# Performance work log

Hardware: AMD Instinct MI355X
Metric: run time of the kernel (lower is better)

Reference implementation:

```python
import jax, jax.numpy as jnp
import numpy as np

LAMBDA_W = 1.0
NEG_INF = -1e10


def setup_inputs() -> dict:
    key = jax.random.key(0)
    k1, k2, k3 = jax.random.split(key, 3)
    B, L, D = 8, 2048, 256
    h_x = jax.random.normal(k1, (B, L, D), dtype=jnp.float32)
    h_y = jax.random.normal(k2, (B, L, D), dtype=jnp.float32)
    # masks: valid prefix of 3/4 length, padded tail of zeros (exercises masking)
    valid = (3 * L) // 4
    base = (jnp.arange(L) < valid).astype(jnp.float32)
    x_mask = jnp.broadcast_to(base, (B, L))
    y_mask = jnp.broadcast_to(base, (B, L))
    # biaffine weight (n_label=1, no biases), init_value scaling kept at O(1)
    W = jax.random.normal(k3, (D, D), dtype=jnp.float32) / jnp.sqrt(jnp.float32(D))
    return {"h_x": h_x, "h_y": h_y, "x_mask": x_mask, "y_mask": y_mask, "W": W}


def reference(h_x, h_y, x_mask, y_mask, W):
    # src = h_x [B,Ls,D], pred = h_y [B,Lp,D]
    src, pred = h_x, h_y
    src_mask, pred_mask = x_mask, y_mask

    # cost_mx[b,p,s] = ||src[b,s] - pred[b,p]||_2, via ||a||^2+||b||^2-2ab
    src_sq = jnp.sum(src * src, axis=-1)            # [B,Ls]
    pred_sq = jnp.sum(pred * pred, axis=-1)         # [B,Lp]
    cross = jnp.einsum('bpd,bsd->bps', pred, src)   # [B,Lp,Ls]
    cost_mx = jnp.sqrt(jnp.maximum(pred_sq[:, :, None] + src_sq[:, None, :] - 2.0 * cross, 0.0))

    # biaffine scores: pred W src^T  -> [B,Lp,Ls]
    tr_mx = jnp.einsum('bpd,de,bse->bps', pred, W, src)

    # cost_mask[b,p,s] = pred_mask[b,p]*src_mask[b,s]
    cost_mask = pred_mask[:, :, None] * src_mask[:, None, :]
    tr_mx = jnp.where(cost_mask == 0, NEG_INF, tr_mx)
    tr_prob = jax.nn.softmax(tr_mx, axis=-1)

    flow_cost = tr_prob * cost_mx                   # [B,Lp,Ls]

    nL1 = jnp.sum(pred_mask, axis=-1, keepdims=True)  # [B,1]
    nL2 = jnp.sum(src_mask, axis=-1, keepdims=True)   # [B,1]
    fc = jnp.sum(flow_cost, axis=(1, 2), keepdims=True)  # [B,1,1]
    fc = fc / (nL1 * nL2)   # broadcasts [B,1,1]/[B,1] -> [B,B,1], matches torch
    fc = jnp.mean(fc)
    return fc * LAMBDA_W
```

## Files before the change

kernel.cpp:

```cpp
#include <hip/hip_runtime.h>
#include <math.h>
#include <stdint.h>

#define B_ 8
#define L_ 2048
#define D_ 256
#define NEG_INF_V (-1e10f)
#define NSTRIP 32

typedef __bf16 bf16x8 __attribute__((ext_vector_type(8)));
typedef float f32x4 __attribute__((ext_vector_type(4)));

#define MFMA16(a, b, c) __builtin_amdgcn_mfma_f32_16x16x32_bf16((a), (b), (c), 0, 0, 0)


__global__ __launch_bounds__(256) void convert_kernel(
    const float* __restrict__ x, const float* __restrict__ y,
    const float* __restrict__ W,
    __bf16* __restrict__ srcFM, __bf16* __restrict__ predFM,
    __bf16* __restrict__ WFM,
    float* __restrict__ src_sq, float* __restrict__ pred_sq) {
    int tid = threadIdx.x;
    int blk = blockIdx.x;
    if (blk < 2048) {
        const float* in = (blk < 1024) ? x : y;
        __bf16* out = (blk < 1024) ? srcFM : predFM;
        float* sqout = (blk < 1024) ? src_sq : pred_sq;
        int g = blk & 1023;
        __shared__ __align__(16) __bf16 sFM[512 * 8];
        __shared__ float sSQ[16];
        int kb = (tid & 31) >> 2, qq = tid & 3;
        #pragma unroll
        for (int pass = 0; pass < 2; ++pass) {
            int m = pass * 8 + (tid >> 5);
            const float* p = in + ((size_t)g * 16 + m) * D_ + (tid & 31) * 8;
            float4 v0 = *(const float4*)p;
            float4 v1 = *(const float4*)(p + 4);
            float ss = v0.x * v0.x + v0.y * v0.y + v0.z * v0.z + v0.w * v0.w +
                       v1.x * v1.x + v1.y * v1.y + v1.z * v1.z + v1.w * v1.w;
            #pragma unroll
            for (int o = 16; o > 0; o >>= 1) ss += __shfl_xor(ss, o, 64);
            if ((tid & 31) == 0) sSQ[m] = ss;
            union { __bf16 o[8]; bf16x8 v; } cv;
            cv.o[0] = (__bf16)v0.x; cv.o[1] = (__bf16)v0.y;
            cv.o[2] = (__bf16)v0.z; cv.o[3] = (__bf16)v0.w;
            cv.o[4] = (__bf16)v1.x; cv.o[5] = (__bf16)v1.y;
            cv.o[6] = (__bf16)v1.z; cv.o[7] = (__bf16)v1.w;
            *(bf16x8*)(sFM + (m * 32 + kb * 4 + qq) * 8) = cv.v;
        }
        __syncthreads();
        int G0 = tid * 2;
        int kb0 = G0 >> 6, q0 = (G0 >> 4) & 3, m0 = G0 & 15;
        bf16x8 a = *(const bf16x8*)(sFM + (m0 * 32 + kb0 * 4 + q0) * 8);
        bf16x8 bgr = *(const bf16x8*)(sFM + ((m0 + 1) * 32 + kb0 * 4 + q0) * 8);
        *(bf16x8*)(out + ((size_t)g * 512 + G0) * 8) = a;
        *(bf16x8*)(out + ((size_t)g * 512 + G0 + 1) * 8) = bgr;
        if (tid < 16) sqout[g * 16 + tid] = sSQ[tid];
    } else {
        int idx = (blk - 2048) * 256 + tid;
        int m = idx & 15, q = (idx >> 4) & 3, kb = (idx >> 6) & 7, gn = idx >> 9;
        union { __bf16 o[8]; bf16x8 v; } cv;
        #pragma unroll
        for (int j = 0; j < 8; ++j)
            cv.o[j] = (__bf16)W[(size_t)(kb * 32 + q * 8 + j) * D_ + gn * 16 + m];
        *(bf16x8*)(WFM + (size_t)idx * 8) = cv.v;
    }
}

__global__ __launch_bounds__(256, 2) void predw_mfma(
    const __bf16* __restrict__ predFM, const __bf16* __restrict__ WFM,
    const float* __restrict__ pred_mask, __bf16* __restrict__ pwFM) {
    __shared__ __align__(16) __bf16 sT[128 * 136];
    __shared__ int flag;
    int tid = threadIdx.x, lane = tid & 63, wid = tid >> 6;
    int wp = wid >> 1, wn = wid & 1;
    int id = blockIdx.x;
    int m0 = (((id >> 3) & 15) + (id & 7) * 16) * 128;
    int n0 = (id >> 7) * 128;
    if (tid == 0) flag = 0;
    __syncthreads();
    if (tid < 128) { if (pred_mask[m0 + tid] != 0.f) atomicOr(&flag, 1); }
    __syncthreads();
    if (!flag) return;

    const __bf16* bA = predFM + (size_t)(m0 / 16 + wp * 4) * 4096 + lane * 8;
    const __bf16* bB = WFM + (size_t)(n0 / 16 + wn * 4) * 4096 + lane * 8;
    f32x4 acc[4][4] = {};
    #pragma unroll
    for (int kb = 0; kb < 8; ++kb) {
        bf16x8 fA[4], fB[4];
        #pragma unroll
        for (int t = 0; t < 4; ++t) {
            fA[t] = *(const bf16x8*)(bA + (t * 8 + kb) * 512);
            fB[t] = *(const bf16x8*)(bB + (t * 8 + kb) * 512);
        }
        #pragma unroll
        for (int pt = 0; pt < 4; ++pt)
            #pragma unroll
            for (int st = 0; st < 4; ++st)
                acc[pt][st] = MFMA16(fA[pt], fB[st], acc[pt][st]);
    }
    int q = lane >> 4, cn = lane & 15;
    #pragma unroll
    for (int pt = 0; pt < 4; ++pt)
        #pragma unroll
        for (int st = 0; st < 4; ++st)
            #pragma unroll
            for (int r = 0; r < 4; ++r)
                sT[(wp * 64 + pt * 16 + q * 4 + r) * 136 + wn * 64 + st * 16 + cn] =
                    (__bf16)acc[pt][st][r];
    __syncthreads();
    #pragma unroll
    for (int i = 0; i < 8; ++i) {
        int idx = i * 256 + tid;
        int gl = idx >> 8, kbl = (idx >> 6) & 3, qq = (idx >> 4) & 3, mm = idx & 15;
        bf16x8 v = *(const bf16x8*)(sT + (gl * 16 + mm) * 136 + kbl * 32 + qq * 8);
        *(bf16x8*)(pwFM +
                   (((size_t)(m0 / 16 + gl) * 8 + n0 / 32 + kbl) * 64 + qq * 16 + mm) * 8) = v;
    }
}

__global__ __launch_bounds__(256, 4) void fused_mfma(
    const __bf16* __restrict__ srcFM, const __bf16* __restrict__ predFM,
    const __bf16* __restrict__ pwFM,
    const float* __restrict__ src_mask, const float* __restrict__ pred_mask,
    const float* __restrict__ src_sq, const float* __restrict__ pred_sq,
    float* __restrict__ m_part, float* __restrict__ l_part,
    float* __restrict__ w_part, float* __restrict__ Sarr,
    unsigned int* __restrict__ counter) {
    __shared__ __align__(16) __bf16 sS[64 * 256];
    __shared__ float sPM[128], sPSQ[128], sSM[64], sSSQ[64];
    __shared__ int flg[4];
    int tid = threadIdx.x, lane = tid & 63, wid = tid >> 6;
    int id = blockIdx.x;
    int b = id & 7, px = (id >> 3) & 15, syb = id >> 7;
    int p0 = px * 128, s0 = syb * 64;

    if (id == 0) {
        if (tid == 0) *counter = 0u;
        if (tid < 24) Sarr[tid] = 0.f;
    }
    if (tid < 4) flg[tid] = 0;
    __syncthreads();
    if (tid < 128) {
        float v = pred_mask[b * L_ + p0 + tid];
        sPM[tid] = v;
        sPSQ[tid] = pred_sq[b * L_ + p0 + tid];
        atomicOr(&flg[(v != 0.f) ? 0 : 1], 1);
    } else if (tid < 192) {
        int t = tid - 128;
        float v = src_mask[b * L_ + s0 + t];
        sSM[t] = v;
        sSSQ[t] = src_sq[b * L_ + s0 + t];
        atomicOr(&flg[(v != 0.f) ? 2 : 3], 1);
    }
    {
        const __bf16* g = srcFM + ((size_t)(b * 128 + syb * 4)) * 4096;
        #pragma unroll
        for (int i = 0; i < 8; ++i) {
            size_t off = (size_t)i * 2048 + tid * 8;
            *(bf16x8*)(sS + off) = *(const bf16x8*)(g + off);
        }
    }
    __syncthreads();
    const bool anyVP = flg[0] != 0, anyIP = flg[1] != 0, anyVS = flg[2] != 0;
    const bool doT = anyVP && anyVS;
    const bool doG = anyVS || anyIP;
    if (!doG) {
        if (tid < 128) {
            size_t o = (size_t)syb * (B_ * L_) + b * L_ + p0 + tid;
            m_part[o] = NEG_INF_V; l_part[o] = 64.f; w_part[o] = 0.f;
        }
        return;
    }

    const __bf16* bP = predFM + ((size_t)(b * 128 + px * 8 + wid * 2)) * 4096 + lane * 8;
    const __bf16* bW = pwFM + ((size_t)(b * 128 + px * 8 + wid * 2)) * 4096 + lane * 8;
    const __bf16* bS = sS + lane * 8;

    f32x4 aG[2][4] = {};
    f32x4 aT[2][4] = {};
    if (doT) {
        #pragma unroll
        for (int kb = 0; kb < 8; ++kb) {
            bf16x8 fP[2], fW[2], fB[4];
            #pragma unroll
            for (int m = 0; m < 2; ++m) {
                fP[m] = *(const bf16x8*)(bP + (m * 8 + kb) * 512);
                fW[m] = *(const bf16x8*)(bW + (m * 8 + kb) * 512);
            }
            #pragma unroll
            for (int t = 0; t < 4; ++t)
                fB[t] = *(const bf16x8*)(bS + (t * 8 + kb) * 512);
            #pragma unroll
            for (int m = 0; m < 2; ++m)
                #pragma unroll
                for (int t = 0; t < 4; ++t) {
                    aG[m][t] = MFMA16(fP[m], fB[t], aG[m][t]);
                    aT[m][t] = MFMA16(fW[m], fB[t], aT[m][t]);
                }
        }
    } else {
        #pragma unroll
        for (int kb = 0; kb < 8; ++kb) {
            bf16x8 fP[2], fB[4];
            #pragma unroll
            for (int m = 0; m < 2; ++m)
                fP[m] = *(const bf16x8*)(bP + (m * 8 + kb) * 512);
            #pragma unroll
            for (int t = 0; t < 4; ++t)
                fB[t] = *(const bf16x8*)(bS + (t * 8 + kb) * 512);
            #pragma unroll
            for (int m = 0; m < 2; ++m)
                #pragma unroll
                for (int t = 0; t < 4; ++t)
                    aG[m][t] = MFMA16(fP[m], fB[t], aG[m][t]);
        }
    }

    int q = lane >> 4, cn = lane & 15;
    float smv[4], sqv[4];
    #pragma unroll
    for (int t = 0; t < 4; ++t) {
        smv[t] = sSM[t * 16 + cn];
        sqv[t] = sSSQ[t * 16 + cn];
    }
    #pragma unroll
    for (int m = 0; m < 2; ++m) {
        int rbase = wid * 32 + m * 16 + q * 4;
        #pragma unroll
        for (int r = 0; r < 4; ++r) {
            float pm = sPM[rbase + r], psq = sPSQ[rbase + r];
            float tv[4], cst[4];
            float tm = -1e30f;
            #pragma unroll
            for (int t = 0; t < 4; ++t) {
                cst[t] = __builtin_amdgcn_sqrtf(
                    fmaxf(psq + sqv[t] - 2.f * aG[m][t][r], 0.f));
                float tt = doT ? aT[m][t][r] : NEG_INF_V;
                tv[t] = (pm == 0.f) ? 0.f : (smv[t] != 0.f ? tt : NEG_INF_V);
                tm = fmaxf(tm, tv[t]);
            }
            #pragma unroll
            for (int o = 8; o > 0; o >>= 1) tm = fmaxf(tm, __shfl_xor(tm, o, 16));
            float l = 0.f, w = 0.f;
            #pragma unroll
            for (int t = 0; t < 4; ++t) {
                float e = __expf(tv[t] - tm);
                l += e;
                w = fmaf(e, cst[t], w);
            }
            #pragma unroll
            for (int o = 8; o > 0; o >>= 1) {
                l += __shfl_xor(l, o, 16);
                w += __shfl_xor(w, o, 16);
            }
            if (cn == 0) {
                size_t o = (size_t)syb * (B_ * L_) + b * L_ + p0 + rbase + r;
                m_part[o] = tm;
                l_part[o] = l;
                w_part[o] = w;
            }
        }
    }
}

__global__ __launch_bounds__(256) void combine_kernel(
    const float* __restrict__ m_part, const float* __restrict__ l_part,
    const float* __restrict__ w_part,
    const float* __restrict__ x_mask, const float* __restrict__ y_mask,
    float* __restrict__ Sarr, unsigned int* __restrict__ counter,
    float* __restrict__ out) {
    int tid = threadIdx.x;
    int r = blockIdx.x * 256 + tid;
    int b = r >> 11;
    float mm = -1e30f;
    #pragma unroll
    for (int s = 0; s < NSTRIP; ++s) mm = fmaxf(mm, m_part[(size_t)s * (B_ * L_) + r]);
    float l = 0.f, w = 0.f;
    #pragma unroll
    for (int s = 0; s < NSTRIP; ++s) {
        size_t o = (size_t)s * (B_ * L_) + r;
        float e = __expf(m_part[o] - mm);
        l = fmaf(l_part[o], e, l);
        w = fmaf(w_part[o], e, w);
    }
    float sv = w / l;
    float n1 = y_mask[r], n2 = x_mask[r];
    __shared__ float red[3][256];
    red[0][tid] = sv; red[1][tid] = n1; red[2][tid] = n2;
    __syncthreads();
    for (int o = 128; o > 0; o >>= 1) {
        if (tid < o) {
            red[0][tid] += red[0][tid + o];
            red[1][tid] += red[1][tid + o];
            red[2][tid] += red[2][tid + o];
        }
        __syncthreads();
    }
    __shared__ int isLast;
    if (tid == 0) {
        atomicAdd(&Sarr[b], red[0][0]);
        atomicAdd(&Sarr[8 + b], red[1][0]);
        atomicAdd(&Sarr[16 + b], red[2][0]);
        __threadfence();
        isLast = (atomicAdd(counter, 1u) == 63u) ? 1 : 0;
    }
    __syncthreads();
    if (isLast) {
        __shared__ float fb[24];
        if (tid < 24) fb[tid] = atomicAdd(&Sarr[tid], 0.f);
        __syncthreads();
        if (tid == 0) {
            float ss = 0.f, si = 0.f;
            for (int bb = 0; bb < B_; bb++) {
                ss += fb[bb];
                si += 1.0f / (fb[8 + bb] * fb[16 + bb]);
            }
            out[0] = ss * si / (float)(B_ * B_);
        }
    }
}

extern "C" void kernel_launch(void* const* d_in, const int* in_sizes, int n_in,
                              void* d_out, int out_size, void* d_ws, size_t ws_size,
                              hipStream_t stream) {
    const float* h_x = (const float*)d_in[0];
    const float* h_y = (const float*)d_in[1];
    const float* x_mask = (const float*)d_in[2];
    const float* y_mask = (const float*)d_in[3];
    const float* W = (const float*)d_in[4];

    char* w8 = (char*)d_ws;
    const size_t BLD2 = (size_t)B_ * L_ * D_ * 2;
    __bf16* srcFM = (__bf16*)w8;
    __bf16* predFM = (__bf16*)(w8 + BLD2);
    __bf16* pwFM = (__bf16*)(w8 + 2 * BLD2);
    __bf16* WFM = (__bf16*)(w8 + 3 * BLD2);
    float* src_sq = (float*)(w8 + 3 * BLD2 + (1 << 17));
    float* pred_sq = (float*)(w8 + 3 * BLD2 + (1 << 17) + (1 << 16));
    char* pbase = w8 + 3 * BLD2 + (1 << 17) + (1 << 17);
    const size_t PSZ = (size_t)B_ * L_ * NSTRIP * 4;
    float* m_part = (float*)pbase;
    float* l_part = (float*)(pbase + PSZ);
    float* w_part = (float*)(pbase + 2 * PSZ);
    float* Sarr = (float*)(pbase + 3 * PSZ);
    unsigned int* counter = (unsigned int*)(pbase + 3 * PSZ + 128);

    convert_kernel<<<2080, 256, 0, stream>>>(h_x, h_y, W, srcFM, predFM, WFM,
                                             src_sq, pred_sq);
    predw_mfma<<<256, 256, 0, stream>>>(predFM, WFM, y_mask, pwFM);
    fused_mfma<<<4096, 256, 0, stream>>>(
        srcFM, predFM, pwFM, x_mask, y_mask, src_sq, pred_sq,
        m_part, l_part, w_part, Sarr, counter);
    combine_kernel<<<B_ * L_ / 256, 256, 0, stream>>>(
        m_part, l_part, w_part, x_mask, y_mask, Sarr, counter, (float*)d_out);
}
```

Before: 137.1 us.

## Precompute src·W^T instead of pred·W and stage it in shared memory

Reassociates the biaffine product so the helper GEMM computes src·Wᵀ (transposed W conversion) rather than pred·W. The fused kernel then keeps both the src tile and the src·Wᵀ tile in LDS and reuses them across a taller 256-row pred tile processed by 512-thread blocks. Only the pred fragments come from global memory. This halves the number of blocks and removes per-wave global loads of the projected tile. The cost is doubled LDS per block (about 64KB), which may reduce occupancy.

```diff
diff --git a/kernel.cpp b/kernel.cpp
--- a/kernel.cpp
+++ b/kernel.cpp
@@ -62,14 +62,14 @@
         union { __bf16 o[8]; bf16x8 v; } cv;
         #pragma unroll
         for (int j = 0; j < 8; ++j)
-            cv.o[j] = (__bf16)W[(size_t)(kb * 32 + q * 8 + j) * D_ + gn * 16 + m];
+            cv.o[j] = (__bf16)W[(size_t)(gn * 16 + m) * D_ + kb * 32 + q * 8 + j];
         *(bf16x8*)(WFM + (size_t)idx * 8) = cv.v;
     }
 }
 
-__global__ __launch_bounds__(256, 2) void predw_mfma(
-    const __bf16* __restrict__ predFM, const __bf16* __restrict__ WFM,
-    const float* __restrict__ pred_mask, __bf16* __restrict__ pwFM) {
+__global__ __launch_bounds__(256, 2) void srcw_mfma(
+    const __bf16* __restrict__ srcFM, const __bf16* __restrict__ WFM,
+    const float* __restrict__ src_mask, __bf16* __restrict__ swFM) {
     __shared__ __align__(16) __bf16 sT[128 * 136];
     __shared__ int flag;
     int tid = threadIdx.x, lane = tid & 63, wid = tid >> 6;
@@ -79,11 +79,11 @@
     int n0 = (id >> 7) * 128;
     if (tid == 0) flag = 0;
     __syncthreads();
-    if (tid < 128) { if (pred_mask[m0 + tid] != 0.f) atomicOr(&flag, 1); }
+    if (tid < 128) { if (src_mask[m0 + tid] != 0.f) atomicOr(&flag, 1); }
     __syncthreads();
     if (!flag) return;
 
-    const __bf16* bA = predFM + (size_t)(m0 / 16 + wp * 4) * 4096 + lane * 8;
+    const __bf16* bA = srcFM + (size_t)(m0 / 16 + wp * 4) * 4096 + lane * 8;
     const __bf16* bB = WFM + (size_t)(n0 / 16 + wn * 4) * 4096 + lane * 8;
     f32x4 acc[4][4] = {};
     #pragma unroll
@@ -115,26 +115,27 @@
         int idx = i * 256 + tid;
         int gl = idx >> 8, kbl = (idx >> 6) & 3, qq = (idx >> 4) & 3, mm = idx & 15;
         bf16x8 v = *(const bf16x8*)(sT + (gl * 16 + mm) * 136 + kbl * 32 + qq * 8);
-        *(bf16x8*)(pwFM +
+        *(bf16x8*)(swFM +
                    (((size_t)(m0 / 16 + gl) * 8 + n0 / 32 + kbl) * 64 + qq * 16 + mm) * 8) = v;
     }
 }
 
-__global__ __launch_bounds__(256, 4) void fused_mfma(
+__global__ __launch_bounds__(512, 4) void fused_mfma(
     const __bf16* __restrict__ srcFM, const __bf16* __restrict__ predFM,
-    const __bf16* __restrict__ pwFM,
+    const __bf16* __restrict__ swFM,
     const float* __restrict__ src_mask, const float* __restrict__ pred_mask,
     const float* __restrict__ src_sq, const float* __restrict__ pred_sq,
     float* __restrict__ m_part, float* __restrict__ l_part,
     float* __restrict__ w_part, float* __restrict__ Sarr,
     unsigned int* __restrict__ counter) {
     __shared__ __align__(16) __bf16 sS[64 * 256];
-    __shared__ float sPM[128], sPSQ[128], sSM[64], sSSQ[64];
+    __shared__ __align__(16) __bf16 sW[64 * 256];
+    __shared__ float sPM[256], sPSQ[256], sSM[64], sSSQ[64];
     __shared__ int flg[4];
     int tid = threadIdx.x, lane = tid & 63, wid = tid >> 6;
     int id = blockIdx.x;
-    int b = id & 7, px = (id >> 3) & 15, syb = id >> 7;
-    int p0 = px * 128, s0 = syb * 64;
+    int b = id & 7, px = (id >> 3) & 7, syb = id >> 6;
+    int p0 = px * 256, s0 = syb * 64;
 
     if (id == 0) {
         if (tid == 0) *counter = 0u;
@@ -142,24 +143,26 @@
     }
     if (tid < 4) flg[tid] = 0;
     __syncthreads();
-    if (tid < 128) {
+    if (tid < 256) {
         float v = pred_mask[b * L_ + p0 + tid];
         sPM[tid] = v;
         sPSQ[tid] = pred_sq[b * L_ + p0 + tid];
         atomicOr(&flg[(v != 0.f) ? 0 : 1], 1);
-    } else if (tid < 192) {
-        int t = tid - 128;
+    } else if (tid < 320) {
+        int t = tid - 256;
         float v = src_mask[b * L_ + s0 + t];
         sSM[t] = v;
         sSSQ[t] = src_sq[b * L_ + s0 + t];
         atomicOr(&flg[(v != 0.f) ? 2 : 3], 1);
     }
     {
-        const __bf16* g = srcFM + ((size_t)(b * 128 + syb * 4)) * 4096;
-        #pragma unroll
-        for (int i = 0; i < 8; ++i) {
-            size_t off = (size_t)i * 2048 + tid * 8;
-            *(bf16x8*)(sS + off) = *(const bf16x8*)(g + off);
+        const __bf16* gS = srcFM + ((size_t)(b * 128 + syb * 4)) * 4096;
+        const __bf16* gW = swFM + ((size_t)(b * 128 + syb * 4)) * 4096;
+        #pragma unroll
+        for (int i = 0; i < 4; ++i) {
+            size_t off = (size_t)i * 4096 + tid * 8;
+            *(bf16x8*)(sS + off) = *(const bf16x8*)(gS + off);
+            *(bf16x8*)(sW + off) = *(const bf16x8*)(gW + off);
         }
     }
     __syncthreads();
@@ -167,38 +170,42 @@
     const bool doT = anyVP && anyVS;
     const bool doG = anyVS || anyIP;
     if (!doG) {
-        if (tid < 128) {
+        if (tid < 256) {
             size_t o = (size_t)syb * (B_ * L_) + b * L_ + p0 + tid;
             m_part[o] = NEG_INF_V; l_part[o] = 64.f; w_part[o] = 0.f;
         }
         return;
     }
 
-    const __bf16* bP = predFM + ((size_t)(b * 128 + px * 8 + wid * 2)) * 4096 + lane * 8;
-    const __bf16* bW = pwFM + ((size_t)(b * 128 + px * 8 + wid * 2)) * 4096 + lane * 8;
+    const __bf16* bP = predFM + ((size_t)(b * 128 + px * 16 + wid * 2)) * 4096 + lane * 8;
     const __bf16* bS = sS + lane * 8;
+    const __bf16* bW = sW + lane * 8;
 
     f32x4 aG[2][4] = {};
     f32x4 aT[2][4] = {};
     if (doT) {
         #pragma unroll
         for (int kb = 0; kb < 8; ++kb) {
-            bf16x8 fP[2], fW[2], fB[4];
-            #pragma unroll
-            for (int m = 0; m < 2; ++m) {
+            bf16x8 fP[2];
+            #pragma unroll
+            for (int m = 0; m < 2; ++m)
                 fP[m] = *(const bf16x8*)(bP + (m * 8 + kb) * 512);
-                fW[m] = *(const bf16x8*)(bW + (m * 8 + kb) * 512);
-            }
-            #pragma unroll
-            for (int t = 0; t < 4; ++t)
-                fB[t] = *(const bf16x8*)(bS + (t * 8 + kb) * 512);
-            #pragma unroll
-            for (int m = 0; m < 2; ++m)
+            #pragma unroll
+            for (int th = 0; th < 2; ++th) {
+                bf16x8 fB[2], fW2[2];
                 #pragma unroll
-                for (int t = 0; t < 4; ++t) {
-                    aG[m][t] = MFMA16(fP[m], fB[t], aG[m][t]);
-                    aT[m][t] = MFMA16(fW[m], fB[t], aT[m][t]);
+                for (int t = 0; t < 2; ++t) {
+                    fB[t] = *(const bf16x8*)(bS + ((th * 2 + t) * 8 + kb) * 512);
+                    fW2[t] = *(const bf16x8*)(bW + ((th * 2 + t) * 8 + kb) * 512);
                 }
+                #pragma unroll
+                for (int m = 0; m < 2; ++m)
+                    #pragma unroll
+                    for (int t = 0; t < 2; ++t) {
+                        aG[m][th * 2 + t] = MFMA16(fP[m], fB[t], aG[m][th * 2 + t]);
+                        aT[m][th * 2 + t] = MFMA16(fP[m], fW2[t], aT[m][th * 2 + t]);
+                    }
+            }
         }
     } else {
         #pragma unroll
@@ -335,7 +342,7 @@
     const size_t BLD2 = (size_t)B_ * L_ * D_ * 2;
     __bf16* srcFM = (__bf16*)w8;
     __bf16* predFM = (__bf16*)(w8 + BLD2);
-    __bf16* pwFM = (__bf16*)(w8 + 2 * BLD2);
+    __bf16* swFM = (__bf16*)(w8 + 2 * BLD2);
     __bf16* WFM = (__bf16*)(w8 + 3 * BLD2);
     float* src_sq = (float*)(w8 + 3 * BLD2 + (1 << 17));
     float* pred_sq = (float*)(w8 + 3 * BLD2 + (1 << 17) + (1 << 16));
@@ -349,9 +356,9 @@
 
     convert_kernel<<<2080, 256, 0, stream>>>(h_x, h_y, W, srcFM, predFM, WFM,
                                              src_sq, pred_sq);
-    predw_mfma<<<256, 256, 0, stream>>>(predFM, WFM, y_mask, pwFM);
-    fused_mfma<<<4096, 256, 0, stream>>>(
-        srcFM, predFM, pwFM, x_mask, y_mask, src_sq, pred_sq,
+    srcw_mfma<<<256, 256, 0, stream>>>(srcFM, WFM, x_mask, swFM);
+    fused_mfma<<<2048, 512, 0, stream>>>(
+        srcFM, predFM, swFM, x_mask, y_mask, src_sq, pred_sq,
         m_part, l_part, w_part, Sarr, counter);
     combine_kernel<<<B_ * L_ / 256, 256, 0, stream>>>(
         m_part, l_part, w_part, x_mask, y_mask, Sarr, counter, (float*)d_out);
```

Measured after the change: 141.0 us. 2.8% more time.

## Fuse combine step into fused_mfma via last-arriving-block counters

Applied to the files above, without the earlier changes.

Removes the separate combine kernel launch. Each (batch, pred-tile) group of 32 strip blocks increments a per-group counter, and the last block to arrive merges the 32 partial softmax statistics for its 128 rows. A second global counter then picks the final block that writes the output. Counters are zeroed with a memset before the kernels run. This saves one kernel launch and its tail, at the cost of extra threadfences and atomics in every block and a serial combine done by a few blocks.

```diff
diff --git a/kernel.cpp b/kernel.cpp
--- a/kernel.cpp
+++ b/kernel.cpp
@@ -126,8 +126,10 @@
     const float* __restrict__ src_mask, const float* __restrict__ pred_mask,
     const float* __restrict__ src_sq, const float* __restrict__ pred_sq,
     float* __restrict__ m_part, float* __restrict__ l_part,
-    float* __restrict__ w_part, float* __restrict__ Sarr,
-    unsigned int* __restrict__ counter) {
+    float* __restrict__ w_part,
+    const float* __restrict__ x_mask, const float* __restrict__ y_mask,
+    float* __restrict__ Sarr, unsigned int* __restrict__ pcnt,
+    unsigned int* __restrict__ fcnt, float* __restrict__ out) {
     __shared__ __align__(16) __bf16 sS[64 * 256];
     __shared__ float sPM[128], sPSQ[128], sSM[64], sSSQ[64];
     __shared__ int flg[4];
@@ -136,10 +138,6 @@
     int b = id & 7, px = (id >> 3) & 15, syb = id >> 7;
     int p0 = px * 128, s0 = syb * 64;
 
-    if (id == 0) {
-        if (tid == 0) *counter = 0u;
-        if (tid < 24) Sarr[tid] = 0.f;
-    }
     if (tid < 4) flg[tid] = 0;
     __syncthreads();
     if (tid < 128) {
@@ -171,143 +169,146 @@
             size_t o = (size_t)syb * (B_ * L_) + b * L_ + p0 + tid;
             m_part[o] = NEG_INF_V; l_part[o] = 64.f; w_part[o] = 0.f;
         }
-        return;
-    }
-
-    const __bf16* bP = predFM + ((size_t)(b * 128 + px * 8 + wid * 2)) * 4096 + lane * 8;
-    const __bf16* bW = pwFM + ((size_t)(b * 128 + px * 8 + wid * 2)) * 4096 + lane * 8;
-    const __bf16* bS = sS + lane * 8;
-
-    f32x4 aG[2][4] = {};
-    f32x4 aT[2][4] = {};
-    if (doT) {
-        #pragma unroll
-        for (int kb = 0; kb < 8; ++kb) {
-            bf16x8 fP[2], fW[2], fB[4];
-            #pragma unroll
-            for (int m = 0; m < 2; ++m) {
-                fP[m] = *(const bf16x8*)(bP + (m * 8 + kb) * 512);
-                fW[m] = *(const bf16x8*)(bW + (m * 8 + kb) * 512);
+    } else {
+        const __bf16* bP = predFM + ((size_t)(b * 128 + px * 8 + wid * 2)) * 4096 + lane * 8;
+        const __bf16* bW = pwFM + ((size_t)(b * 128 + px * 8 + wid * 2)) * 4096 + lane * 8;
+        const __bf16* bS = sS + lane * 8;
+
+        f32x4 aG[2][4] = {};
+        f32x4 aT[2][4] = {};
+        if (doT) {
+            #pragma unroll
+            for (int kb = 0; kb < 8; ++kb) {
+                bf16x8 fP[2], fW[2], fB[4];
+                #pragma unroll
+                for (int m = 0; m < 2; ++m) {
+                    fP[m] = *(const bf16x8*)(bP + (m * 8 + kb) * 512);
+                    fW[m] = *(const bf16x8*)(bW + (m * 8 + kb) * 512);
+                }
+                #pragma unroll
+                for (int t = 0; t < 4; ++t)
+                    fB[t] = *(const bf16x8*)(bS + (t * 8 + kb) * 512);
+                #pragma unroll
+                for (int m = 0; m < 2; ++m)
+                    #pragma unroll
+                    for (int t = 0; t < 4; ++t) {
+                        aG[m][t] = MFMA16(fP[m], fB[t], aG[m][t]);
+                        aT[m][t] = MFMA16(fW[m], fB[t], aT[m][t]);
+                    }
             }
-            #pragma unroll
-            for (int t = 0; t < 4; ++t)
-                fB[t] = *(const bf16x8*)(bS + (t * 8 + kb) * 512);
-            #pragma unroll
-            for (int m = 0; m < 2; ++m)
+        } else {
+            #pragma unroll
+            for (int kb = 0; kb < 8; ++kb) {
+                bf16x8 fP[2], fB[4];
+                #pragma unroll
+                for (int m = 0; m < 2; ++m)
+                    fP[m] = *(const bf16x8*)(bP + (m * 8 + kb) * 512);
+                #pragma unroll
+                for (int t = 0; t < 4; ++t)
+                    fB[t] = *(const bf16x8*)(bS + (t * 8 + kb) * 512);
+                #pragma unroll
+                for (int m = 0; m < 2; ++m)
+                    #pragma unroll
+                    for (int t = 0; t < 4; ++t)
+                        aG[m][t] = MFMA16(fP[m], fB[t], aG[m][t]);
+            }
+        }
+
+        int q = lane >> 4, cn = lane & 15;
+        float smv[4], sqv[4];
+        #pragma unroll
+        for (int t = 0; t < 4; ++t) {
+            smv[t] = sSM[t * 16 + cn];
+            sqv[t] = sSSQ[t * 16 + cn];
+        }
+        #pragma unroll
+        for (int m = 0; m < 2; ++m) {
+            int rbase = wid * 32 + m * 16 + q * 4;
+            #pragma unroll
+            for (int r = 0; r < 4; ++r) {
+                float pm = sPM[rbase + r], psq = sPSQ[rbase + r];
+                float tv[4], cst[4];
+                float tm = -1e30f;
                 #pragma unroll
                 for (int t = 0; t < 4; ++t) {
-                    aG[m][t] = MFMA16(fP[m], fB[t], aG[m][t]);
-                    aT[m][t] = MFMA16(fW[m], fB[t], aT[m][t]);
-                }
-        }
-    } else {
-        #pragma unroll
-        for (int kb = 0; kb < 8; ++kb) {
-            bf16x8 fP[2], fB[4];
-            #pragma unroll
-            for (int m = 0; m < 2; ++m)
-                fP[m] = *(const bf16x8*)(bP + (m * 8 + kb) * 512);
-            #pragma unroll
-            for (int t = 0; t < 4; ++t)
-                fB[t] = *(const bf16x8*)(bS + (t * 8 + kb) * 512);
-            #pragma unroll
-            for (int m = 0; m < 2; ++m)
-                #pragma unroll
-                for (int t = 0; t < 4; ++t)
-                    aG[m][t] = MFMA16(fP[m], fB[t], aG[m][t]);
-        }
-    }
-
-    int q = lane >> 4, cn = lane & 15;
-    float smv[4], sqv[4];
-    #pragma unroll
-    for (int t = 0; t < 4; ++t) {
-        smv[t] = sSM[t * 16 + cn];
-        sqv[t] = sSSQ[t * 16 + cn];
-    }
-    #pragma unroll
-    for (int m = 0; m < 2; ++m) {
-        int rbase = wid * 32 + m * 16 + q * 4;
-        #pragma unroll
-        for (int r = 0; r < 4; ++r) {
-            float pm = sPM[rbase + r], psq = sPSQ[rbase + r];
-            float tv[4], cst[4];
-            float tm = -1e30f;
-            #pragma unroll
-            for (int t = 0; t < 4; ++t) {
-                cst[t] = __builtin_amdgcn_sqrtf(
-                    fmaxf(psq + sqv[t] - 2.f * aG[m][t][r], 0.f));
-                float tt = doT ? aT[m][t][r] : NEG_INF_V;
-                tv[t] = (pm == 0.f) ? 0.f : (smv[t] != 0.f ? tt : NEG_INF_V);
-                tm = fmaxf(tm, tv[t]);
+                    cst[t] = __builtin_amdgcn_sqrtf(
+                        fmaxf(psq + sqv[t] - 2.f * aG[m][t][r], 0.f));
+                    float tt = doT ? aT[m][t][r] : NEG_INF_V;
+                    tv[t] = (pm == 0.f) ? 0.f : (smv[t] != 0.f ? tt : NEG_INF_V);
+                    tm = fmaxf(tm, tv[t]);
+                }
+                #pragma unroll
+                for (int o = 8; o > 0; o >>= 1) tm = fmaxf(tm, __shfl_xor(tm, o, 16));
+                float l = 0.f, w = 0.f;
+                #pragma unroll
+                for (int t = 0; t < 4; ++t) {
+                    float e = __expf(tv[t] - tm);
+                    l += e;
+                    w = fmaf(e, cst[t], w);
+                }
+                #pragma unroll
+                for (int o = 8; o > 0; o >>= 1) {
+                    l += __shfl_xor(l, o, 16);
+                    w += __shfl_xor(w, o, 16);
+                }
+                if (cn == 0) {
+                    size_t o = (size_t)syb * (B_ * L_) + b * L_ + p0 + rbase + r;
+                    m_part[o] = tm;
+                    l_part[o] = l;
+                    w_part[o] = w;
+                }
             }
-            #pragma unroll
-            for (int o = 8; o > 0; o >>= 1) tm = fmaxf(tm, __shfl_xor(tm, o, 16));
-            float l = 0.f, w = 0.f;
-            #pragma unroll
-            for (int t = 0; t < 4; ++t) {
-                float e = __expf(tv[t] - tm);
-                l += e;
-                w = fmaf(e, cst[t], w);
-            }
-            #pragma unroll
-            for (int o = 8; o > 0; o >>= 1) {
-                l += __shfl_xor(l, o, 16);
-                w += __shfl_xor(w, o, 16);
-            }
-            if (cn == 0) {
-                size_t o = (size_t)syb * (B_ * L_) + b * L_ + p0 + rbase + r;
-                m_part[o] = tm;
-                l_part[o] = l;
-                w_part[o] = w;
-            }
-        }
-    }
-}
-
-__global__ __launch_bounds__(256) void combine_kernel(
-    const float* __restrict__ m_part, const float* __restrict__ l_part,
-    const float* __restrict__ w_part,
-    const float* __restrict__ x_mask, const float* __restrict__ y_mask,
-    float* __restrict__ Sarr, unsigned int* __restrict__ counter,
-    float* __restrict__ out) {
-    int tid = threadIdx.x;
-    int r = blockIdx.x * 256 + tid;
-    int b = r >> 11;
-    float mm = -1e30f;
-    #pragma unroll
-    for (int s = 0; s < NSTRIP; ++s) mm = fmaxf(mm, m_part[(size_t)s * (B_ * L_) + r]);
-    float l = 0.f, w = 0.f;
-    #pragma unroll
-    for (int s = 0; s < NSTRIP; ++s) {
-        size_t o = (size_t)s * (B_ * L_) + r;
-        float e = __expf(m_part[o] - mm);
-        l = fmaf(l_part[o], e, l);
-        w = fmaf(w_part[o], e, w);
-    }
-    float sv = w / l;
-    float n1 = y_mask[r], n2 = x_mask[r];
-    __shared__ float red[3][256];
-    red[0][tid] = sv; red[1][tid] = n1; red[2][tid] = n2;
+        }
+    }
+
+    __threadfence();
+    __shared__ int comb;
+    if (tid == 0)
+        comb = (atomicAdd(&pcnt[b * 16 + px], 1u) == 31u) ? 1 : 0;
+    __syncthreads();
+    if (!comb) return;
+    __threadfence();
+
+    float sv = 0.f, n1 = 0.f, n2 = 0.f;
+    if (tid < 128) {
+        int r = b * L_ + p0 + tid;
+        float mm = -1e30f;
+        #pragma unroll
+        for (int s = 0; s < NSTRIP; ++s)
+            mm = fmaxf(mm, m_part[(size_t)s * (B_ * L_) + r]);
+        float l = 0.f, w = 0.f;
+        #pragma unroll 8
+        for (int s = 0; s < NSTRIP; ++s) {
+            size_t o = (size_t)s * (B_ * L_) + r;
+            float e = __expf(m_part[o] - mm);
+            l = fmaf(l_part[o], e, l);
+            w = fmaf(w_part[o], e, w);
+        }
+        sv = w / l;
+        n1 = y_mask[r];
+        n2 = x_mask[r];
+    }
+    float* red = (float*)sS;
+    red[tid] = sv; red[256 + tid] = n1; red[512 + tid] = n2;
     __syncthreads();
     for (int o = 128; o > 0; o >>= 1) {
         if (tid < o) {
-            red[0][tid] += red[0][tid + o];
-            red[1][tid] += red[1][tid + o];
-            red[2][tid] += red[2][tid + o];
+            red[tid] += red[tid + o];
+            red[256 + tid] += red[256 + tid + o];
+            red[512 + tid] += red[512 + tid + o];
         }
         __syncthreads();
     }
-    __shared__ int isLast;
+    __shared__ int lastf;
     if (tid == 0) {
-        atomicAdd(&Sarr[b], red[0][0]);
-        atomicAdd(&Sarr[8 + b], red[1][0]);
-        atomicAdd(&Sarr[16 + b], red[2][0]);
+        atomicAdd(&Sarr[b], red[0]);
+        atomicAdd(&Sarr[8 + b], red[256]);
+        atomicAdd(&Sarr[16 + b], red[512]);
         __threadfence();
-        isLast = (atomicAdd(counter, 1u) == 63u) ? 1 : 0;
-    }
-    __syncthreads();
-    if (isLast) {
+        lastf = (atomicAdd(fcnt, 1u) == 127u) ? 1 : 0;
+    }
+    __syncthreads();
+    if (lastf) {
         __shared__ float fb[24];
         if (tid < 24) fb[tid] = atomicAdd(&Sarr[tid], 0.f);
         __syncthreads();
@@ -344,15 +345,17 @@
     float* m_part = (float*)pbase;
     float* l_part = (float*)(pbase + PSZ);
     float* w_part = (float*)(pbase + 2 * PSZ);
-    float* Sarr = (float*)(pbase + 3 * PSZ);
-    unsigned int* counter = (unsigned int*)(pbase + 3 * PSZ + 128);
-
+    char* ctrl = pbase + 3 * PSZ;
+    float* Sarr = (float*)ctrl;
+    unsigned int* pcnt = (unsigned int*)(ctrl + 128);
+    unsigned int* fcnt = (unsigned int*)(ctrl + 128 + 512);
+
+    hipMemsetAsync(ctrl, 0, 1024, stream);
     convert_kernel<<<2080, 256, 0, stream>>>(h_x, h_y, W, srcFM, predFM, WFM,
                                              src_sq, pred_sq);
     predw_mfma<<<256, 256, 0, stream>>>(predFM, WFM, y_mask, pwFM);
     fused_mfma<<<4096, 256, 0, stream>>>(
         srcFM, predFM, pwFM, x_mask, y_mask, src_sq, pred_sq,
-        m_part, l_part, w_part, Sarr, counter);
-    combine_kernel<<<B_ * L_ / 256, 256, 0, stream>>>(
-        m_part, l_part, w_part, x_mask, y_mask, Sarr, counter, (float*)d_out);
+        m_part, l_part, w_part, x_mask, y_mask, Sarr, pcnt, fcnt,
+        (float*)d_out);
 }
```

New measurement: 485.1 us. 3.54x slower.

## Fuse pred conversion into pred·W GEMM kernel, keeping pred tile in LDS

Applied to the files above, without the earlier changes.

Pred fp32-to-bf16 conversion and squared-norm computation move out of the convert kernel into the pred·W MFMA kernel. Each block converts a 64-row pred tile into LDS, writes predFM to global for later use, and computes the full 256-wide output from LDS. This drops the global re-read of predFM and shrinks the convert launch. The cost is smaller GEMM tiles (64x256 per block) with W re-read from global by every block, plus extra syncs around a two-phase transpose.

```diff
diff --git a/kernel.cpp b/kernel.cpp
--- a/kernel.cpp
+++ b/kernel.cpp
@@ -15,25 +15,20 @@
 
 
 __global__ __launch_bounds__(256) void convert_kernel(
-    const float* __restrict__ x, const float* __restrict__ y,
-    const float* __restrict__ W,
-    __bf16* __restrict__ srcFM, __bf16* __restrict__ predFM,
-    __bf16* __restrict__ WFM,
-    float* __restrict__ src_sq, float* __restrict__ pred_sq) {
+    const float* __restrict__ x, const float* __restrict__ W,
+    __bf16* __restrict__ srcFM, __bf16* __restrict__ WFM,
+    float* __restrict__ src_sq) {
     int tid = threadIdx.x;
     int blk = blockIdx.x;
-    if (blk < 2048) {
-        const float* in = (blk < 1024) ? x : y;
-        __bf16* out = (blk < 1024) ? srcFM : predFM;
-        float* sqout = (blk < 1024) ? src_sq : pred_sq;
-        int g = blk & 1023;
+    if (blk < 1024) {
+        int g = blk;
         __shared__ __align__(16) __bf16 sFM[512 * 8];
         __shared__ float sSQ[16];
         int kb = (tid & 31) >> 2, qq = tid & 3;
         #pragma unroll
         for (int pass = 0; pass < 2; ++pass) {
             int m = pass * 8 + (tid >> 5);
-            const float* p = in + ((size_t)g * 16 + m) * D_ + (tid & 31) * 8;
+            const float* p = x + ((size_t)g * 16 + m) * D_ + (tid & 31) * 8;
             float4 v0 = *(const float4*)p;
             float4 v1 = *(const float4*)(p + 4);
             float ss = v0.x * v0.x + v0.y * v0.y + v0.z * v0.z + v0.w * v0.w +
@@ -53,11 +48,11 @@
         int kb0 = G0 >> 6, q0 = (G0 >> 4) & 3, m0 = G0 & 15;
         bf16x8 a = *(const bf16x8*)(sFM + (m0 * 32 + kb0 * 4 + q0) * 8);
         bf16x8 bgr = *(const bf16x8*)(sFM + ((m0 + 1) * 32 + kb0 * 4 + q0) * 8);
-        *(bf16x8*)(out + ((size_t)g * 512 + G0) * 8) = a;
-        *(bf16x8*)(out + ((size_t)g * 512 + G0 + 1) * 8) = bgr;
-        if (tid < 16) sqout[g * 16 + tid] = sSQ[tid];
+        *(bf16x8*)(srcFM + ((size_t)g * 512 + G0) * 8) = a;
+        *(bf16x8*)(srcFM + ((size_t)g * 512 + G0 + 1) * 8) = bgr;
+        if (tid < 16) src_sq[g * 16 + tid] = sSQ[tid];
     } else {
-        int idx = (blk - 2048) * 256 + tid;
+        int idx = (blk - 1024) * 256 + tid;
         int m = idx & 15, q = (idx >> 4) & 3, kb = (idx >> 6) & 7, gn = idx >> 9;
         union { __bf16 o[8]; bf16x8 v; } cv;
         #pragma unroll
@@ -67,56 +62,91 @@
     }
 }
 
-__global__ __launch_bounds__(256, 2) void predw_mfma(
-    const __bf16* __restrict__ predFM, const __bf16* __restrict__ WFM,
-    const float* __restrict__ pred_mask, __bf16* __restrict__ pwFM) {
-    __shared__ __align__(16) __bf16 sT[128 * 136];
+__global__ __launch_bounds__(256, 4) void predconv_predw(
+    const float* __restrict__ y, const __bf16* __restrict__ WFM,
+    const float* __restrict__ pred_mask,
+    __bf16* __restrict__ predFM, float* __restrict__ pred_sq,
+    __bf16* __restrict__ pwFM) {
+    __shared__ __align__(16) __bf16 sP[64 * 264];
     __shared__ int flag;
     int tid = threadIdx.x, lane = tid & 63, wid = tid >> 6;
+    int id = blockIdx.x;
+    int b = id & 7, t8 = id >> 3;
+    int g1 = b * 32 + t8;
+    size_t R0 = (size_t)g1 * 64;
+    if (tid == 0) flag = 0;
+    __syncthreads();
+    if (tid < 64) { if (pred_mask[R0 + tid] != 0.f) atomicOr(&flag, 1); }
+
+    int q = lane >> 4, m = lane & 15;
+    float ss = 0.f;
+    const float* yb = y + (R0 + wid * 16 + m) * D_ + q * 8;
+    __bf16* pfb = predFM + (((size_t)(g1 * 4 + wid) * 8) * 64 + lane) * 8;
+    #pragma unroll
+    for (int kb = 0; kb < 8; ++kb) {
+        float4 v0 = *(const float4*)(yb + kb * 32);
+        float4 v1 = *(const float4*)(yb + kb * 32 + 4);
+        ss += v0.x * v0.x + v0.y * v0.y + v0.z * v0.z + v0.w * v0.w +
+              v1.x * v1.x + v1.y * v1.y + v1.z * v1.z + v1.w * v1.w;
+        union { __bf16 o[8]; bf16x8 v; } cv;
+        cv.o[0] = (__bf16)v0.x; cv.o[1] = (__bf16)v0.y;
+        cv.o[2] = (__bf16)v0.z; cv.o[3] = (__bf16)v0.w;
+        cv.o[4] = (__bf16)v1.x; cv.o[5] = (__bf16)v1.y;
+        cv.o[6] = (__bf16)v1.z; cv.o[7] = (__bf16)v1.w;
+        *(bf16x8*)(sP + ((wid * 8 + kb) * 64 + lane) * 8) = cv.v;
+        *(bf16x8*)(pfb + (size_t)kb * 512) = cv.v;
+    }
+    ss += __shfl_xor(ss, 16, 64);
+    ss += __shfl_xor(ss, 32, 64);
+    if (q == 0) pred_sq[R0 + wid * 16 + m] = ss;
+    __syncthreads();
+    if (!flag) return;
+
     int wp = wid >> 1, wn = wid & 1;
-    int id = blockIdx.x;
-    int m0 = (((id >> 3) & 15) + (id & 7) * 16) * 128;
-    int n0 = (id >> 7) * 128;
-    if (tid == 0) flag = 0;
-    __syncthreads();
-    if (tid < 128) { if (pred_mask[m0 + tid] != 0.f) atomicOr(&flag, 1); }
-    __syncthreads();
-    if (!flag) return;
-
-    const __bf16* bA = predFM + (size_t)(m0 / 16 + wp * 4) * 4096 + lane * 8;
-    const __bf16* bB = WFM + (size_t)(n0 / 16 + wn * 4) * 4096 + lane * 8;
-    f32x4 acc[4][4] = {};
+    f32x4 acc[2][8] = {};
+    const __bf16* bB = WFM + ((size_t)(wn * 8) * 8 * 64 + lane) * 8;
     #pragma unroll
     for (int kb = 0; kb < 8; ++kb) {
-        bf16x8 fA[4], fB[4];
-        #pragma unroll
-        for (int t = 0; t < 4; ++t) {
-            fA[t] = *(const bf16x8*)(bA + (t * 8 + kb) * 512);
-            fB[t] = *(const bf16x8*)(bB + (t * 8 + kb) * 512);
-        }
-        #pragma unroll
-        for (int pt = 0; pt < 4; ++pt)
-            #pragma unroll
-            for (int st = 0; st < 4; ++st)
-                acc[pt][st] = MFMA16(fA[pt], fB[st], acc[pt][st]);
-    }
-    int q = lane >> 4, cn = lane & 15;
-    #pragma unroll
-    for (int pt = 0; pt < 4; ++pt)
-        #pragma unroll
-        for (int st = 0; st < 4; ++st)
-            #pragma unroll
-            for (int r = 0; r < 4; ++r)
-                sT[(wp * 64 + pt * 16 + q * 4 + r) * 136 + wn * 64 + st * 16 + cn] =
-                    (__bf16)acc[pt][st][r];
-    __syncthreads();
-    #pragma unroll
-    for (int i = 0; i < 8; ++i) {
-        int idx = i * 256 + tid;
-        int gl = idx >> 8, kbl = (idx >> 6) & 3, qq = (idx >> 4) & 3, mm = idx & 15;
-        bf16x8 v = *(const bf16x8*)(sT + (gl * 16 + mm) * 136 + kbl * 32 + qq * 8);
-        *(bf16x8*)(pwFM +
-                   (((size_t)(m0 / 16 + gl) * 8 + n0 / 32 + kbl) * 64 + qq * 16 + mm) * 8) = v;
+        bf16x8 fA[2];
+        #pragma unroll
+        for (int a = 0; a < 2; ++a)
+            fA[a] = *(const bf16x8*)(sP + (((wp * 2 + a) * 8 + kb) * 64 + lane) * 8);
+        #pragma unroll
+        for (int h = 0; h < 2; ++h) {
+            bf16x8 fB[4];
+            #pragma unroll
+            for (int t = 0; t < 4; ++t)
+                fB[t] = *(const bf16x8*)(bB + ((size_t)((h * 4 + t) * 8 + kb) * 64) * 8);
+            #pragma unroll
+            for (int a = 0; a < 2; ++a)
+                #pragma unroll
+                for (int t = 0; t < 4; ++t)
+                    acc[a][h * 4 + t] = MFMA16(fA[a], fB[t], acc[a][h * 4 + t]);
+        }
+    }
+    int cn = lane & 15;
+    #pragma unroll
+    for (int h = 0; h < 2; ++h) {
+        __syncthreads();
+        if (wn == h) {
+            #pragma unroll
+            for (int a = 0; a < 2; ++a)
+                #pragma unroll
+                for (int t = 0; t < 8; ++t)
+                    #pragma unroll
+                    for (int r = 0; r < 4; ++r)
+                        sP[(wp * 32 + a * 16 + q * 4 + r) * 136 + t * 16 + cn] =
+                            (__bf16)acc[a][t][r];
+        }
+        __syncthreads();
+        #pragma unroll
+        for (int i = 0; i < 4; ++i) {
+            int idx = i * 256 + tid;
+            int G = idx >> 8, kbl = (idx >> 6) & 3, qq = (idx >> 4) & 3, mm = idx & 15;
+            bf16x8 v = *(const bf16x8*)(sP + (G * 16 + mm) * 136 + kbl * 32 + qq * 8);
+            *(bf16x8*)(pwFM +
+                       (((size_t)(g1 * 4 + G) * 8 + h * 4 + kbl) * 64 + qq * 16 + mm) * 8) = v;
+        }
     }
 }
 
@@ -347,9 +377,9 @@
     float* Sarr = (float*)(pbase + 3 * PSZ);
     unsigned int* counter = (unsigned int*)(pbase + 3 * PSZ + 128);
 
-    convert_kernel<<<2080, 256, 0, stream>>>(h_x, h_y, W, srcFM, predFM, WFM,
-                                             src_sq, pred_sq);
-    predw_mfma<<<256, 256, 0, stream>>>(predFM, WFM, y_mask, pwFM);
+    convert_kernel<<<1056, 256, 0, stream>>>(h_x, W, srcFM, WFM, src_sq);
+    predconv_predw<<<256, 256, 0, stream>>>(h_y, WFM, y_mask, predFM, pred_sq,
+                                            pwFM);
     fused_mfma<<<4096, 256, 0, stream>>>(
         srcFM, predFM, pwFM, x_mask, y_mask, src_sq, pred_sq,
         m_part, l_part, w_part, Sarr, counter);
```

Result: no change. 139.6 us (+1.8%).
